# Optimization experiments

Measured on AMD Instinct MI355X. Metric: run time of the kernel, lower is better.

The kernel has to match this reference:

```python
import jax, jax.numpy as jnp
import numpy as np

NUM_HEADS = 16
HEAD_DIM = 128
ROPE_BASE = 10000.0


def _rotate_half(x):
    x1, x2 = jnp.split(x, 2, axis=-1)
    return jnp.concatenate([-x2, x1], axis=-1)


def setup_inputs() -> dict:
    key = jax.random.key(0)
    ks = jax.random.split(key, 6)
    B, S, H = 2, 2048, 2048
    hidden_states = jax.random.normal(ks[0], (B, S, H), dtype=jnp.float32)
    # causal additive mask: 0 on/below diagonal, large negative above
    causal = jnp.tril(jnp.ones((S, S), dtype=bool))
    attention_mask = jnp.where(causal, 0.0, -1e9).astype(jnp.float32)[None, None]
    position_ids = jnp.broadcast_to(jnp.arange(S, dtype=jnp.int64), (B, S))
    sc = 1.0 / np.sqrt(H)
    Wq = jax.random.normal(ks[1], (H, H), dtype=jnp.float32) * sc
    Wk = jax.random.normal(ks[2], (H, H), dtype=jnp.float32) * sc
    Wv = jax.random.normal(ks[3], (H, H), dtype=jnp.float32) * sc
    Wo = jax.random.normal(ks[4], (H, H), dtype=jnp.float32) * sc
    return {"hidden_states": hidden_states, "attention_mask": attention_mask,
            "position_ids": position_ids, "Wq": Wq, "Wk": Wk, "Wv": Wv, "Wo": Wo}


def reference(hidden_states, attention_mask, position_ids, Wq, Wk, Wv, Wo):
    B, S, H = hidden_states.shape
    nH, hd = NUM_HEADS, HEAD_DIM
    # projections (torch Linear: x @ W.T)
    q = (hidden_states @ Wq.T).reshape(B, S, nH, hd).transpose(0, 2, 1, 3)  # [B,nH,S,hd]
    k = (hidden_states @ Wk.T).reshape(B, S, nH, hd).transpose(0, 2, 1, 3)
    v = (hidden_states @ Wv.T).reshape(B, S, nH, hd).transpose(0, 2, 1, 3)
    # rotary embeddings: cos/sin cache over positions, duplicated to full head_dim
    inv_freq = 1.0 / (ROPE_BASE ** (jnp.arange(0, hd, 2, dtype=jnp.float32) / hd))  # [hd/2]
    t = jnp.arange(S, dtype=jnp.float32)
    freqs = jnp.outer(t, inv_freq)                       # [S, hd/2]
    emb = jnp.concatenate([freqs, freqs], axis=-1)       # [S, hd]
    cos = jnp.cos(emb)[position_ids][:, None]            # [B,1,S,hd]
    sin = jnp.sin(emb)[position_ids][:, None]
    q = q * cos + _rotate_half(q) * sin
    k = k * cos + _rotate_half(k) * sin
    # eager attention
    scores = jnp.einsum('bhqd,bhkd->bhqk', q, k) / np.sqrt(hd).astype(np.float32)
    scores = scores + attention_mask
    attn = jax.nn.softmax(scores, axis=-1)
    out = jnp.einsum('bhqk,bhkd->bhqd', attn, v)         # [B,nH,S,hd]
    out = out.transpose(0, 2, 1, 3).reshape(B, S, H)
    return out @ Wo.T
```

## Files before the change

### kernel.cpp

```cpp
#include <hip/hip_runtime.h>
#include <cstdint>
#include <cstddef>

#define NH    16
#define HD    128
#define SEQ   2048
#define HID   2048
#define BATCH 2
#define MTOT  (BATCH*SEQ)

#define SCALE 0.08838834764831845f
#define L2E   1.4426950408889634f
#define KSCL  (0.08838834764831845f * 1.4426950408889634f)
#define L2_10K_D64 0.20762050593046458f

typedef __bf16 bf16x8 __attribute__((ext_vector_type(8)));
typedef float  floatx4 __attribute__((ext_vector_type(4)));

__device__ __forceinline__ unsigned short f2bf(float f) {
  union { float f; unsigned u; } v; v.f = f;
  unsigned u = v.u;
  return (unsigned short)((u + 0x7FFFu + ((u >> 16) & 1u)) >> 16);
}
__device__ __forceinline__ float bf2f(unsigned short h) {
  union { unsigned u; float f; } v; v.u = ((unsigned)h) << 16; return v.f;
}

__device__ __forceinline__ void gld16(const unsigned short* g, unsigned short* l) {
  auto gp = reinterpret_cast<const __attribute__((address_space(1))) void*>(
      reinterpret_cast<uintptr_t>(g));
  auto lp = reinterpret_cast<__attribute__((address_space(3))) void*>(
      reinterpret_cast<uintptr_t>(l));
  __builtin_amdgcn_global_load_lds(gp, lp, 16, 0, 0);
}

__global__ void cvt_all(const float* __restrict__ X,
                        const float* __restrict__ Wq, const float* __restrict__ Wk,
                        const float* __restrict__ Wv, const float* __restrict__ Wo,
                        unsigned short* __restrict__ Xb,
                        unsigned short* __restrict__ Wqb, unsigned short* __restrict__ Wkb,
                        unsigned short* __restrict__ Wvb, unsigned short* __restrict__ Wob) {
  int i = blockIdx.x * blockDim.x + threadIdx.x;
  const float* src; unsigned short* dst; int k;
  if (i < (1 << 21)) { src = X; dst = Xb; k = i; }
  else {
    int j = i - (1 << 21);
    int seg = j >> 20; k = j & ((1 << 20) - 1);
    src = (seg == 0) ? Wq : (seg == 1) ? Wk : (seg == 2) ? Wv : Wo;
    dst = (seg == 0) ? Wqb : (seg == 1) ? Wkb : (seg == 2) ? Wvb : Wob;
  }
  float4 v = reinterpret_cast<const float4*>(src)[k];
  ushort4 o;
  o.x = f2bf(v.x); o.y = f2bf(v.y); o.z = f2bf(v.z); o.w = f2bf(v.w);
  reinterpret_cast<ushort4*>(dst)[k] = o;
}

__global__ void rope_qk(unsigned short* __restrict__ Q,
                        unsigned short* __restrict__ Kk) {
  int idx = blockIdx.x * blockDim.x + threadIdx.x;
  if (idx >= BATCH * NH * SEQ * 64) return;
  int i  = idx & 63;
  int s  = (idx >> 6) & (SEQ - 1);
  int bh = idx >> 17;
  float freq = exp2f(-(float)i * L2_10K_D64);
  float th = (float)s * freq;
  float cx = cosf(th), sy = sinf(th);
  size_t base = ((size_t)bh * SEQ + s) * HD;
  float qa = bf2f(Q[base + i]), qb = bf2f(Q[base + i + 64]);
  Q[base + i]      = f2bf(qa * cx - qb * sy);
  Q[base + i + 64] = f2bf(qb * cx + qa * sy);
  float ka = bf2f(Kk[base + i]), kb = bf2f(Kk[base + i + 64]);
  Kk[base + i]      = f2bf(ka * cx - kb * sy);
  Kk[base + i + 64] = f2bf(kb * cx + ka * sy);
}


#define SBAR      asm volatile("s_barrier" ::: "memory")
#define WAITLGKM  asm volatile("s_waitcnt lgkmcnt(0)" ::: "memory")
#define WAITVM(n) asm volatile("s_waitcnt vmcnt(" #n ")" ::: "memory")
#define PRIO1     __builtin_amdgcn_s_setprio(1)
#define PRIO0     __builtin_amdgcn_s_setprio(0)

#define STAGE(gptr, sptr, buf, half, t8)                                        \
  {                                                                             \
    _Pragma("unroll")                                                           \
    for (int j_ = 0; j_ < 2; ++j_) {                                            \
      int G_   = j_ * 512 + tid;                                                \
      int row_ = G_ >> 3;                                                       \
      int cgs_ = (G_ & 7) ^ (row_ & 7);                                         \
      gld16(gptr + (size_t)((half) * 128 + row_) * HID + (t8) * 64 + cgs_ * 8,  \
            sptr + (buf) * 16384 + (half) * 8192 + G_ * 8);                     \
    }                                                                           \
  }

#define LDA(buf, qm)                                                            \
  _Pragma("unroll")                                                             \
  for (int mr_ = 0; mr_ < 4; ++mr_)                                             \
    _Pragma("unroll")                                                           \
    for (int ks_ = 0; ks_ < 2; ++ks_)                                           \
      af[mr_][ks_] = *reinterpret_cast<const bf16x8*>(                          \
          &As[(buf) * 16384 + (wm * 128 + (qm) * 64 + mr_ * 16 + l16) * 64 + cgo[ks_]]);

#define LDB2(buf, nr0)                                                          \
  _Pragma("unroll")                                                             \
  for (int nr_ = 0; nr_ < 2; ++nr_)                                             \
    _Pragma("unroll")                                                           \
    for (int ks_ = 0; ks_ < 2; ++ks_)                                           \
      bfr[(nr0) + nr_][ks_] = *reinterpret_cast<const bf16x8*>(                 \
          &Bs[(buf) * 16384 + (wn * 64 + ((nr0) + nr_) * 16 + l16) * 64 + cgo[ks_]]);

#define MM(qm, qn)                                                              \
  _Pragma("unroll")                                                             \
  for (int ks_ = 0; ks_ < 2; ++ks_)                                             \
    _Pragma("unroll")                                                           \
    for (int mr_ = 0; mr_ < 4; ++mr_)                                           \
      _Pragma("unroll")                                                         \
      for (int nr_ = 0; nr_ < 2; ++nr_)                                         \
        acc[(qm) * 4 + mr_][(qn) * 2 + nr_] =                                   \
            __builtin_amdgcn_mfma_f32_16x16x32_bf16(                            \
                af[mr_][ks_], bfr[(qn) * 2 + nr_][ks_],                         \
                acc[(qm) * 4 + mr_][(qn) * 2 + nr_], 0, 0, 0);

__global__ __launch_bounds__(512)
void gemm_qkv256(const unsigned short* __restrict__ Xb,
                 const unsigned short* __restrict__ Wq,
                 const unsigned short* __restrict__ Wk,
                 const unsigned short* __restrict__ Wv,
                 unsigned short* __restrict__ Qo,
                 unsigned short* __restrict__ Ko,
                 unsigned short* __restrict__ Vto) {
  __shared__ unsigned short As[2 * 16384];
  __shared__ unsigned short Bs[2 * 16384];

  const int z = blockIdx.z;
  const unsigned short* W = (z == 0) ? Wq : (z == 1) ? Wk : Wv;
  const int mBase = blockIdx.y * 256, nBase = blockIdx.x * 256;
  const unsigned short* Ag = Xb + (size_t)mBase * HID;
  const unsigned short* Bg = W  + (size_t)nBase * HID;

  const int tid  = threadIdx.x;
  const int wave = tid >> 6, lane = tid & 63;
  const int l16  = lane & 15, quad = lane >> 4;
  const int wm   = wave >> 2, wn = wave & 3;
  const int xr   = l16 & 7;
  const int cgo[2] = { ((quad) ^ xr) * 8, ((quad + 4) ^ xr) * 8 };

  floatx4 acc[8][4];
#pragma unroll
  for (int i = 0; i < 8; ++i)
#pragma unroll
    for (int j = 0; j < 4; ++j) acc[i][j] = {0.f, 0.f, 0.f, 0.f};

  bf16x8 af[4][2], bfr[4][2];

  STAGE(Bg, Bs, 0, 0, 0); STAGE(Bg, Bs, 0, 1, 0);
  STAGE(Ag, As, 0, 0, 0); STAGE(Ag, As, 0, 1, 0);
  STAGE(Bg, Bs, 1, 0, 1); STAGE(Bg, Bs, 1, 1, 1);
  WAITVM(4);
  SBAR;

#pragma unroll 1
  for (int i = 0; i < 15; ++i) {
    const int t = 2 * i;
    LDA(0, 0); LDB2(0, 0);
    STAGE(Ag, As, 1, 0, t + 1);
    SBAR; WAITLGKM; PRIO1; MM(0, 0); PRIO0; SBAR;
    LDB2(0, 2);
    STAGE(Ag, As, 1, 1, t + 1);
    SBAR; WAITLGKM; PRIO1; MM(0, 1); PRIO0; SBAR;
    LDA(0, 1);
    STAGE(Bg, Bs, 0, 0, t + 2);
    SBAR; WAITLGKM; PRIO1; MM(1, 0); PRIO0; SBAR;
    STAGE(Bg, Bs, 0, 1, t + 2);
    SBAR; PRIO1; MM(1, 1); PRIO0; WAITVM(4); SBAR;
    LDA(1, 0); LDB2(1, 0);
    STAGE(Ag, As, 0, 0, t + 2);
    SBAR; WAITLGKM; PRIO1; MM(0, 0); PRIO0; SBAR;
    LDB2(1, 2);
    STAGE(Ag, As, 0, 1, t + 2);
    SBAR; WAITLGKM; PRIO1; MM(0, 1); PRIO0; SBAR;
    LDA(1, 1);
    STAGE(Bg, Bs, 1, 0, t + 3);
    SBAR; WAITLGKM; PRIO1; MM(1, 0); PRIO0; SBAR;
    STAGE(Bg, Bs, 1, 1, t + 3);
    SBAR; PRIO1; MM(1, 1); PRIO0; WAITVM(4); SBAR;
  }

  LDA(0, 0); LDB2(0, 0);
  STAGE(Ag, As, 1, 0, 31);
  SBAR; WAITLGKM; PRIO1; MM(0, 0); PRIO0; SBAR;
  LDB2(0, 2);
  STAGE(Ag, As, 1, 1, 31);
  SBAR; WAITLGKM; PRIO1; MM(0, 1); PRIO0; SBAR;
  LDA(0, 1);
  SBAR; WAITLGKM; PRIO1; MM(1, 0); PRIO0; SBAR;
  SBAR; PRIO1; MM(1, 1); PRIO0; WAITVM(0); SBAR;
  LDA(1, 0); LDB2(1, 0);
  SBAR; WAITLGKM; PRIO1; MM(0, 0); PRIO0; SBAR;
  LDB2(1, 2);
  SBAR; WAITLGKM; PRIO1; MM(0, 1); PRIO0; SBAR;
  LDA(1, 1);
  SBAR; WAITLGKM; PRIO1; MM(1, 0); MM(1, 1); PRIO0;

#pragma unroll
  for (int mr = 0; mr < 8; ++mr) {
    int mrow = mBase + wm * 128 + mr * 16 + quad * 4;
#pragma unroll
    for (int nr = 0; nr < 4; ++nr) {
      int n = nBase + wn * 64 + nr * 16 + l16;
      int hh = n >> 7, d = n & 127;
      if (z < 2) {
        unsigned short* dst = (z == 0) ? Qo : Ko;
#pragma unroll
        for (int r = 0; r < 4; ++r) {
          int m = mrow + r;
          int bb = m >> 11, s = m & (SEQ - 1);
          dst[(((size_t)bb * NH + hh) * SEQ + s) * HD + d] = f2bf(acc[mr][nr][r]);
        }
      } else {
        int bb = mrow >> 11, s = mrow & (SEQ - 1);
        ushort4 pk;
        pk.x = f2bf(acc[mr][nr][0]); pk.y = f2bf(acc[mr][nr][1]);
        pk.z = f2bf(acc[mr][nr][2]); pk.w = f2bf(acc[mr][nr][3]);
        *reinterpret_cast<ushort4*>(&Vto[(((size_t)bb * NH + hh) * HD + d) * SEQ + s]) = pk;
      }
    }
  }
}

__device__ __forceinline__ void gemm_core(const unsigned short* __restrict__ A,
                                          const unsigned short* __restrict__ B,
                                          int K, int mBase, int nBase,
                                          unsigned short* As, unsigned short* Bs,
                                          floatx4 acc[4][4]) {
  int tid  = threadIdx.x;
  int wave = tid >> 6, lane = tid & 63;
  int l16  = lane & 15, quad = lane >> 4;
  int wm   = wave >> 1, wn = wave & 1;

  const unsigned short* Ag = A + (size_t)mBase * K;
  const unsigned short* Bg = B + (size_t)nBase * K;

  for (int k0 = 0; k0 < K; k0 += 32) {
    __syncthreads();
#pragma unroll
    for (int r = 0; r < 2; ++r) {
      int row0 = wave * 32 + r * 16;
      int grow = row0 + (lane >> 2);
      int gcol = k0 + (lane & 3) * 8;
      gld16(Ag + (size_t)grow * K + gcol, As + row0 * 32 + lane * 8);
      gld16(Bg + (size_t)grow * K + gcol, Bs + row0 * 32 + lane * 8);
    }
    __syncthreads();

    bf16x8 af[4], bfr[4];
#pragma unroll
    for (int t = 0; t < 4; ++t) {
      af[t]  = *reinterpret_cast<const bf16x8*>(&As[(wm * 64 + t * 16 + l16) * 32 + quad * 8]);
      bfr[t] = *reinterpret_cast<const bf16x8*>(&Bs[(wn * 64 + t * 16 + l16) * 32 + quad * 8]);
    }
#pragma unroll
    for (int tm = 0; tm < 4; ++tm)
#pragma unroll
      for (int tn = 0; tn < 4; ++tn)
        acc[tm][tn] = __builtin_amdgcn_mfma_f32_16x16x32_bf16(af[tm], bfr[tn], acc[tm][tn], 0, 0, 0);
  }
}

__global__ __launch_bounds__(256)
void gemm_out(const unsigned short* __restrict__ Ob,
              const unsigned short* __restrict__ Wo,
              float* __restrict__ out) {
  __shared__ unsigned short As[128 * 32];
  __shared__ unsigned short Bs[128 * 32];
  int mBase = blockIdx.y * 128, nBase = blockIdx.x * 128;

  floatx4 acc[4][4];
#pragma unroll
  for (int i = 0; i < 4; ++i)
#pragma unroll
    for (int j = 0; j < 4; ++j) acc[i][j] = {0.f, 0.f, 0.f, 0.f};

  gemm_core(Ob, Wo, HID, mBase, nBase, As, Bs, acc);

  int tid = threadIdx.x;
  int wave = tid >> 6, lane = tid & 63;
  int l16 = lane & 15, quad = lane >> 4;
  int wm = wave >> 1, wn = wave & 1;

#pragma unroll
  for (int tm = 0; tm < 4; ++tm) {
    int mrow = mBase + wm * 64 + tm * 16 + quad * 4;
#pragma unroll
    for (int tn = 0; tn < 4; ++tn) {
      int n = nBase + wn * 64 + tn * 16 + l16;
#pragma unroll
      for (int r = 0; r < 4; ++r)
        out[(size_t)(mrow + r) * HID + n] = acc[tm][tn][r];
    }
  }
}

__global__ __launch_bounds__(512)
void attn_kernel(const unsigned short* __restrict__ Q,
                 const unsigned short* __restrict__ K,
                 const unsigned short* __restrict__ Vt,
                 unsigned short* __restrict__ Ob) {
  __shared__ unsigned short Ks[32 * 136];
  __shared__ unsigned short Vs[128 * 40];
  __shared__ unsigned short Ps[8][16 * 40];

  int qt = 15 - blockIdx.y;
  int bh = blockIdx.x;
  int b = bh >> 4, h = bh & 15;
  int q0 = qt * 128;
  int tid = threadIdx.x;
  int wave = tid >> 6, lane = tid & 63;
  int l16 = lane & 15, quad = lane >> 4;

  const size_t headQ = (size_t)bh * SEQ * HD;
  const size_t headV = (size_t)bh * HD * SEQ;

  bf16x8 qf[4];
  {
    int qrow = q0 + wave * 16 + l16;
    const unsigned short* qp = Q + headQ + (size_t)qrow * HD + quad * 8;
#pragma unroll
    for (int c = 0; c < 4; ++c)
      qf[c] = *reinterpret_cast<const bf16x8*>(qp + c * 32);
  }

  floatx4 oacc[8];
#pragma unroll
  for (int i = 0; i < 8; ++i) oacc[i] = {0.f, 0.f, 0.f, 0.f};
  float rs[4];
#pragma unroll
  for (int r = 0; r < 4; ++r) rs[r] = 0.f;

  int qq = q0 + wave * 16 + quad * 4;
  int qmax = q0 + wave * 16 + 15;
  unsigned short* pw = Ps[wave];

  int nkt = q0 / 32 + 4;
  for (int kt = 0; kt < nkt; ++kt) {
    int k0 = kt * 32;
    __syncthreads();
    {
      int row = tid >> 4, dc = (tid & 15) * 8;
      *reinterpret_cast<uint4*>(&Ks[row * 136 + dc]) =
        *reinterpret_cast<const uint4*>(&K[headQ + (size_t)(k0 + row) * HD + dc]);
    }
    {
      int row = tid >> 2, kc = (tid & 3) * 8;
      *reinterpret_cast<uint4*>(&Vs[row * 40 + kc]) =
        *reinterpret_cast<const uint4*>(&Vt[headV + (size_t)row * SEQ + k0 + kc]);
    }
    __syncthreads();

    if (k0 <= qmax) {
      floatx4 sc[2];
#pragma unroll
      for (int nt = 0; nt < 2; ++nt) {
        floatx4 s4 = {0.f, 0.f, 0.f, 0.f};
#pragma unroll
        for (int c = 0; c < 4; ++c) {
          bf16x8 kf = *reinterpret_cast<const bf16x8*>(&Ks[(nt * 16 + l16) * 136 + c * 32 + quad * 8]);
          s4 = __builtin_amdgcn_mfma_f32_16x16x32_bf16(qf[c], kf, s4, 0, 0, 0);
        }
        sc[nt] = s4;
      }

#pragma unroll
      for (int nt = 0; nt < 2; ++nt) {
        int kk = k0 + nt * 16 + l16;
#pragma unroll
        for (int r = 0; r < 4; ++r) {
          float arg = (kk <= qq + r) ? fmaf(sc[nt][r], KSCL, -32.0f) : -1e9f;
          float p = exp2f(arg);
          rs[r] += p;
          pw[(quad * 4 + r) * 40 + nt * 16 + l16] = f2bf(p);
        }
      }
      __asm__ __volatile__("s_waitcnt lgkmcnt(0)" ::: "memory");
      bf16x8 pf = *reinterpret_cast<const bf16x8*>(&pw[l16 * 40 + quad * 8]);

#pragma unroll
      for (int dt = 0; dt < 8; ++dt) {
        bf16x8 vf = *reinterpret_cast<const bf16x8*>(&Vs[(dt * 16 + l16) * 40 + quad * 8]);
        oacc[dt] = __builtin_amdgcn_mfma_f32_16x16x32_bf16(pf, vf, oacc[dt], 0, 0, 0);
      }
    }
  }

#pragma unroll
  for (int off = 1; off < 16; off <<= 1)
#pragma unroll
    for (int r = 0; r < 4; ++r) rs[r] += __shfl_xor(rs[r], off, 16);

  float inv[4];
#pragma unroll
  for (int r = 0; r < 4; ++r) inv[r] = 1.0f / rs[r];
#pragma unroll
  for (int dt = 0; dt < 8; ++dt)
#pragma unroll
    for (int r = 0; r < 4; ++r) {
      int s = q0 + wave * 16 + quad * 4 + r;
      Ob[(((size_t)b * SEQ + s) * NH + h) * HD + dt * 16 + l16] = f2bf(oacc[dt][r] * inv[r]);
    }
}

extern "C" void kernel_launch(void* const* d_in, const int* in_sizes, int n_in,
                              void* d_out, int out_size, void* d_ws, size_t ws_size,
                              hipStream_t stream) {
  const float* X  = (const float*)d_in[0];
  const float* Wq = (const float*)d_in[3];
  const float* Wk = (const float*)d_in[4];
  const float* Wv = (const float*)d_in[5];
  const float* Wo = (const float*)d_in[6];

  char* w = (char*)d_ws;
  size_t off = 0;
  auto alloc = [&](size_t bytes) { char* p = w + off; off += (bytes + 255) & ~(size_t)255; return p; };

  unsigned short* Xb  = (unsigned short*)alloc((size_t)MTOT * HID * 2);
  unsigned short* Wqb = (unsigned short*)alloc((size_t)HID * HID * 2);
  unsigned short* Wkb = (unsigned short*)alloc((size_t)HID * HID * 2);
  unsigned short* Wvb = (unsigned short*)alloc((size_t)HID * HID * 2);
  unsigned short* Wob = (unsigned short*)alloc((size_t)HID * HID * 2);
  unsigned short* Qb  = (unsigned short*)alloc((size_t)BATCH * NH * SEQ * HD * 2);
  unsigned short* Kb  = (unsigned short*)alloc((size_t)BATCH * NH * SEQ * HD * 2);
  unsigned short* Vtb = (unsigned short*)alloc((size_t)BATCH * NH * HD * SEQ * 2);
  unsigned short* Obf = (unsigned short*)alloc((size_t)BATCH * SEQ * NH * HD * 2);

  const int nAll4 = (MTOT * HID + 4 * HID * HID) / 4;
  cvt_all<<<nAll4 / 256, 256, 0, stream>>>(X, Wq, Wk, Wv, Wo, Xb, Wqb, Wkb, Wvb, Wob);

  gemm_qkv256<<<dim3(HID / 256, MTOT / 256, 3), 512, 0, stream>>>(Xb, Wqb, Wkb, Wvb, Qb, Kb, Vtb);

  rope_qk<<<(BATCH * NH * SEQ * 64) / 256, 256, 0, stream>>>(Qb, Kb);

  attn_kernel<<<dim3(BATCH * NH, SEQ / 128), 512, 0, stream>>>(Qb, Kb, Vtb, Obf);

  gemm_out<<<dim3(HID / 128, MTOT / 128), 256, 0, stream>>>(Obf, Wob, (float*)d_out);
}
```

Baseline: 409.1 us.

## Fuse RoPE into QKV GEMM epilogue with a column remap and a precomputed cos/sin table

Removes the separate rope_qk pass. RoPE is applied in the QKV GEMM epilogue, using a new B-tile column mapping so each lane holds both the d and d+64 elements, plus a small precomputed cos/sin table. The change also flattens the grid with a block swizzle across 8 groups, likely for XCD/L2 locality, and adds sched_barrier fences before the MFMA bursts and a launch-bounds occupancy hint. The cost is an extra small table kernel and table loads in the epilogue, while a full read-modify-write pass over Q and K disappears.

```diff
diff --git a/kernel.cpp b/kernel.cpp
--- a/kernel.cpp
+++ b/kernel.cpp
@@ -32,6 +32,14 @@
   auto lp = reinterpret_cast<__attribute__((address_space(3))) void*>(
       reinterpret_cast<uintptr_t>(l));
   __builtin_amdgcn_global_load_lds(gp, lp, 16, 0, 0);
+}
+
+__global__ void rope_tab(float2* __restrict__ T) {
+  int idx = blockIdx.x * blockDim.x + threadIdx.x;
+  int s = idx >> 6, i = idx & 63;
+  float freq = exp2f(-(float)i * L2_10K_D64);
+  float th = (float)s * freq;
+  T[idx] = make_float2(cosf(th), sinf(th));
 }
 
 __global__ void cvt_all(const float* __restrict__ X,
@@ -55,31 +63,13 @@
   reinterpret_cast<ushort4*>(dst)[k] = o;
 }
 
-__global__ void rope_qk(unsigned short* __restrict__ Q,
-                        unsigned short* __restrict__ Kk) {
-  int idx = blockIdx.x * blockDim.x + threadIdx.x;
-  if (idx >= BATCH * NH * SEQ * 64) return;
-  int i  = idx & 63;
-  int s  = (idx >> 6) & (SEQ - 1);
-  int bh = idx >> 17;
-  float freq = exp2f(-(float)i * L2_10K_D64);
-  float th = (float)s * freq;
-  float cx = cosf(th), sy = sinf(th);
-  size_t base = ((size_t)bh * SEQ + s) * HD;
-  float qa = bf2f(Q[base + i]), qb = bf2f(Q[base + i + 64]);
-  Q[base + i]      = f2bf(qa * cx - qb * sy);
-  Q[base + i + 64] = f2bf(qb * cx + qa * sy);
-  float ka = bf2f(Kk[base + i]), kb = bf2f(Kk[base + i + 64]);
-  Kk[base + i]      = f2bf(ka * cx - kb * sy);
-  Kk[base + i + 64] = f2bf(kb * cx + ka * sy);
-}
-
 
 #define SBAR      asm volatile("s_barrier" ::: "memory")
 #define WAITLGKM  asm volatile("s_waitcnt lgkmcnt(0)" ::: "memory")
 #define WAITVM(n) asm volatile("s_waitcnt vmcnt(" #n ")" ::: "memory")
 #define PRIO1     __builtin_amdgcn_s_setprio(1)
 #define PRIO0     __builtin_amdgcn_s_setprio(0)
+#define SCHED0    __builtin_amdgcn_sched_barrier(0)
 
 #define STAGE(gptr, sptr, buf, half, t8)                                        \
   {                                                                             \
@@ -107,7 +97,7 @@
     _Pragma("unroll")                                                           \
     for (int ks_ = 0; ks_ < 2; ++ks_)                                           \
       bfr[(nr0) + nr_][ks_] = *reinterpret_cast<const bf16x8*>(                 \
-          &Bs[(buf) * 16384 + (wn * 64 + ((nr0) + nr_) * 16 + l16) * 64 + cgo[ks_]]);
+          &Bs[(buf) * 16384 + (((nr0) + nr_) * 64 + wn * 16 + l16) * 64 + cgo[ks_]]);
 
 #define MM(qm, qn)                                                              \
   _Pragma("unroll")                                                             \
@@ -121,20 +111,27 @@
                 af[mr_][ks_], bfr[(qn) * 2 + nr_][ks_],                         \
                 acc[(qm) * 4 + mr_][(qn) * 2 + nr_], 0, 0, 0);
 
-__global__ __launch_bounds__(512)
+__global__ __launch_bounds__(512, 2)
 void gemm_qkv256(const unsigned short* __restrict__ Xb,
                  const unsigned short* __restrict__ Wq,
                  const unsigned short* __restrict__ Wk,
                  const unsigned short* __restrict__ Wv,
+                 const float2* __restrict__ ropeT,
                  unsigned short* __restrict__ Qo,
                  unsigned short* __restrict__ Ko,
                  unsigned short* __restrict__ Vto) {
   __shared__ unsigned short As[2 * 16384];
   __shared__ unsigned short Bs[2 * 16384];
 
-  const int z = blockIdx.z;
+  const int bid  = blockIdx.x;
+  const int flat = (bid & 7) * 48 + (bid >> 3);
+  const int by   = flat / 24;
+  const int r2   = flat - by * 24;
+  const int z    = r2 >> 3;
+  const int bx   = r2 & 7;
+
   const unsigned short* W = (z == 0) ? Wq : (z == 1) ? Wk : Wv;
-  const int mBase = blockIdx.y * 256, nBase = blockIdx.x * 256;
+  const int mBase = by * 256, nBase = bx * 256;
   const unsigned short* Ag = Xb + (size_t)mBase * HID;
   const unsigned short* Bg = W  + (size_t)nBase * HID;
 
@@ -164,61 +161,73 @@
     const int t = 2 * i;
     LDA(0, 0); LDB2(0, 0);
     STAGE(Ag, As, 1, 0, t + 1);
-    SBAR; WAITLGKM; PRIO1; MM(0, 0); PRIO0; SBAR;
+    SBAR; WAITLGKM; SCHED0; PRIO1; MM(0, 0); PRIO0; SBAR;
     LDB2(0, 2);
     STAGE(Ag, As, 1, 1, t + 1);
-    SBAR; WAITLGKM; PRIO1; MM(0, 1); PRIO0; SBAR;
+    SBAR; WAITLGKM; SCHED0; PRIO1; MM(0, 1); PRIO0; SBAR;
     LDA(0, 1);
     STAGE(Bg, Bs, 0, 0, t + 2);
-    SBAR; WAITLGKM; PRIO1; MM(1, 0); PRIO0; SBAR;
+    SBAR; WAITLGKM; SCHED0; PRIO1; MM(1, 0); PRIO0; SBAR;
     STAGE(Bg, Bs, 0, 1, t + 2);
-    SBAR; PRIO1; MM(1, 1); PRIO0; WAITVM(4); SBAR;
+    SBAR; SCHED0; PRIO1; MM(1, 1); PRIO0; WAITVM(4); SBAR;
     LDA(1, 0); LDB2(1, 0);
     STAGE(Ag, As, 0, 0, t + 2);
-    SBAR; WAITLGKM; PRIO1; MM(0, 0); PRIO0; SBAR;
+    SBAR; WAITLGKM; SCHED0; PRIO1; MM(0, 0); PRIO0; SBAR;
     LDB2(1, 2);
     STAGE(Ag, As, 0, 1, t + 2);
-    SBAR; WAITLGKM; PRIO1; MM(0, 1); PRIO0; SBAR;
+    SBAR; WAITLGKM; SCHED0; PRIO1; MM(0, 1); PRIO0; SBAR;
     LDA(1, 1);
     STAGE(Bg, Bs, 1, 0, t + 3);
-    SBAR; WAITLGKM; PRIO1; MM(1, 0); PRIO0; SBAR;
+    SBAR; WAITLGKM; SCHED0; PRIO1; MM(1, 0); PRIO0; SBAR;
     STAGE(Bg, Bs, 1, 1, t + 3);
-    SBAR; PRIO1; MM(1, 1); PRIO0; WAITVM(4); SBAR;
+    SBAR; SCHED0; PRIO1; MM(1, 1); PRIO0; WAITVM(4); SBAR;
   }
 
   LDA(0, 0); LDB2(0, 0);
   STAGE(Ag, As, 1, 0, 31);
-  SBAR; WAITLGKM; PRIO1; MM(0, 0); PRIO0; SBAR;
+  SBAR; WAITLGKM; SCHED0; PRIO1; MM(0, 0); PRIO0; SBAR;
   LDB2(0, 2);
   STAGE(Ag, As, 1, 1, 31);
-  SBAR; WAITLGKM; PRIO1; MM(0, 1); PRIO0; SBAR;
+  SBAR; WAITLGKM; SCHED0; PRIO1; MM(0, 1); PRIO0; SBAR;
   LDA(0, 1);
-  SBAR; WAITLGKM; PRIO1; MM(1, 0); PRIO0; SBAR;
-  SBAR; PRIO1; MM(1, 1); PRIO0; WAITVM(0); SBAR;
+  SBAR; WAITLGKM; SCHED0; PRIO1; MM(1, 0); PRIO0; SBAR;
+  SBAR; SCHED0; PRIO1; MM(1, 1); PRIO0; WAITVM(0); SBAR;
   LDA(1, 0); LDB2(1, 0);
-  SBAR; WAITLGKM; PRIO1; MM(0, 0); PRIO0; SBAR;
+  SBAR; WAITLGKM; SCHED0; PRIO1; MM(0, 0); PRIO0; SBAR;
   LDB2(1, 2);
-  SBAR; WAITLGKM; PRIO1; MM(0, 1); PRIO0; SBAR;
+  SBAR; WAITLGKM; SCHED0; PRIO1; MM(0, 1); PRIO0; SBAR;
   LDA(1, 1);
-  SBAR; WAITLGKM; PRIO1; MM(1, 0); MM(1, 1); PRIO0;
-
-#pragma unroll
-  for (int mr = 0; mr < 8; ++mr) {
-    int mrow = mBase + wm * 128 + mr * 16 + quad * 4;
-#pragma unroll
-    for (int nr = 0; nr < 4; ++nr) {
-      int n = nBase + wn * 64 + nr * 16 + l16;
-      int hh = n >> 7, d = n & 127;
-      if (z < 2) {
-        unsigned short* dst = (z == 0) ? Qo : Ko;
-#pragma unroll
-        for (int r = 0; r < 4; ++r) {
-          int m = mrow + r;
-          int bb = m >> 11, s = m & (SEQ - 1);
-          dst[(((size_t)bb * NH + hh) * SEQ + s) * HD + d] = f2bf(acc[mr][nr][r]);
+  SBAR; WAITLGKM; SCHED0; PRIO1; MM(1, 0); MM(1, 1); PRIO0;
+
+  if (z < 2) {
+    unsigned short* dst = (z == 0) ? Qo : Ko;
+    const int hh0 = nBase >> 7;
+    const int d1  = wn * 16 + l16;
+#pragma unroll
+    for (int mr = 0; mr < 8; ++mr) {
+      int srow = mBase + wm * 128 + mr * 16 + quad * 4;
+      int bb = srow >> 11, s = srow & (SEQ - 1);
+#pragma unroll
+      for (int r = 0; r < 4; ++r) {
+        float2 cs = ropeT[(size_t)(s + r) * 64 + d1];
+#pragma unroll
+        for (int p = 0; p < 2; ++p) {
+          float x1 = acc[mr][2 * p][r], x2 = acc[mr][2 * p + 1][r];
+          size_t base = (((size_t)bb * NH + hh0 + p) * SEQ + (s + r)) * HD;
+          dst[base + d1]      = f2bf(x1 * cs.x - x2 * cs.y);
+          dst[base + d1 + 64] = f2bf(x2 * cs.x + x1 * cs.y);
         }
-      } else {
-        int bb = mrow >> 11, s = mrow & (SEQ - 1);
+      }
+    }
+  } else {
+#pragma unroll
+    for (int mr = 0; mr < 8; ++mr) {
+      int mrow = mBase + wm * 128 + mr * 16 + quad * 4;
+      int bb = mrow >> 11, s = mrow & (SEQ - 1);
+#pragma unroll
+      for (int nr = 0; nr < 4; ++nr) {
+        int n = nBase + nr * 64 + wn * 16 + l16;
+        int hh = n >> 7, d = n & 127;
         ushort4 pk;
         pk.x = f2bf(acc[mr][nr][0]); pk.y = f2bf(acc[mr][nr][1]);
         pk.z = f2bf(acc[mr][nr][2]); pk.w = f2bf(acc[mr][nr][3]);
@@ -431,13 +440,14 @@
   unsigned short* Kb  = (unsigned short*)alloc((size_t)BATCH * NH * SEQ * HD * 2);
   unsigned short* Vtb = (unsigned short*)alloc((size_t)BATCH * NH * HD * SEQ * 2);
   unsigned short* Obf = (unsigned short*)alloc((size_t)BATCH * SEQ * NH * HD * 2);
+  float2*         ropeT = (float2*)alloc((size_t)SEQ * 64 * sizeof(float2));
+
+  rope_tab<<<(SEQ * 64) / 256, 256, 0, stream>>>(ropeT);
 
   const int nAll4 = (MTOT * HID + 4 * HID * HID) / 4;
   cvt_all<<<nAll4 / 256, 256, 0, stream>>>(X, Wq, Wk, Wv, Wo, Xb, Wqb, Wkb, Wvb, Wob);
 
-  gemm_qkv256<<<dim3(HID / 256, MTOT / 256, 3), 512, 0, stream>>>(Xb, Wqb, Wkb, Wvb, Qb, Kb, Vtb);
-
-  rope_qk<<<(BATCH * NH * SEQ * 64) / 256, 256, 0, stream>>>(Qb, Kb);
+  gemm_qkv256<<<384, 512, 0, stream>>>(Xb, Wqb, Wkb, Wvb, ropeT, Qb, Kb, Vtb);
 
   attn_kernel<<<dim3(BATCH * NH, SEQ / 128), 512, 0, stream>>>(Qb, Kb, Vtb, Obf);
 
```

Measured after the change: 403.6 us. About the same (-1.3%).
